# Performance work log

Measured on AMD Instinct MI355X. Metric: run time of the kernel, lower is better.

Reference implementation:

```python
import jax, jax.numpy as jnp
import numpy as np

B, S, E = 2, 2048, 2048
H, HKV, KQV = 16, 4, 2048
D = KQV // H            # 128 head dim
KV_DIM = D * HKV        # 512
WINDOW = 256
NEG = jnp.finfo(jnp.float32).min


def setup_inputs() -> dict:
    key = jax.random.key(0)
    ks = jax.random.split(key, 5)
    sc = 0.02
    return {
        "hidden_states": jax.random.normal(ks[0], (B, S, E), jnp.float32),
        "Wq": jax.random.normal(ks[1], (KQV, E), jnp.float32) * sc,
        "Wk": jax.random.normal(ks[2], (KV_DIM, E), jnp.float32) * sc,
        "Wv": jax.random.normal(ks[3], (KV_DIM, E), jnp.float32) * sc,
        "Wo": jax.random.normal(ks[4], (E, KQV), jnp.float32) * sc,
        "bo": jnp.zeros((E,), jnp.float32),
    }


def reference(hidden_states, Wq, Wk, Wv, Wo, bo):
    x = hidden_states
    # projections (nn.Linear: x @ W.T)
    q = (x @ Wq.T).reshape(B, S, H, D).transpose(0, 2, 1, 3)      # [B,H,S,D]
    k = (x @ Wk.T).reshape(B, S, HKV, D).transpose(0, 2, 1, 3)    # [B,HKV,S,D]
    v = (x @ Wv.T).reshape(B, S, HKV, D).transpose(0, 2, 1, 3)

    # faithful reproduction of the module's index_select head expansion:
    # group_sizes are uniform (H % HKV == 0); both query and kv indices are
    # [0]*g + [1]*g + ... so query head i (i < HKV) is duplicated g times.
    idx = jnp.repeat(jnp.arange(HKV), H // HKV)                   # [H]
    qs = q[:, idx]                                                # [B,H,S,D]
    ks = k[:, idx]
    vs = v[:, idx]

    # GPT-Neo style: no 1/sqrt(D) scaling
    scores = jnp.einsum('bhqd,bhkd->bhqk', qs, ks)                # [B,H,S,S]

    i = jnp.arange(S)[:, None]
    j = jnp.arange(S)[None, :]
    # local causal mask: j <= i and j > i - WINDOW
    mask = (j <= i) & (j > i - WINDOW)                            # [S,S]
    scores = jnp.where(mask[None, None], scores, NEG)
    attn = jax.nn.softmax(scores, axis=-1)

    out = jnp.einsum('bhqk,bhkd->bhqd', attn, vs)                 # [B,H,S,D]
    out = out.transpose(0, 2, 1, 3).reshape(B, S, H * D)          # merge heads
    return out @ Wo.T + bo
```

## Files before the change

kernel.cpp:

```cpp
#include <hip/hip_runtime.h>

typedef _Float16 f16;
typedef _Float16 f16x8 __attribute__((ext_vector_type(8)));
typedef _Float16 f16x4 __attribute__((ext_vector_type(4)));
typedef float    f32x4 __attribute__((ext_vector_type(4)));


__device__ __forceinline__ void load_lds16(const void* g, void* l) {
    __builtin_amdgcn_global_load_lds(
        (__attribute__((address_space(1))) void*)(g),
        (__attribute__((address_space(3))) void*)(l), 16, 0, 0);
}

__global__ __launch_bounds__(256)
void cvt_pack(const float* __restrict__ X, const float* __restrict__ Wq,
              const float* __restrict__ Wk, const float* __restrict__ Wv,
              const float* __restrict__ Wo,
              f16* __restrict__ Xp, f16* __restrict__ Wp, f16* __restrict__ Wrp)
{
    const int blk = blockIdx.x, tid = threadIdx.x;
    if (blk < 4096) {
        int cid = blk * 256 + tid;
        int tile = cid >> 8, wc = cid & 255;
        int row = wc >> 2, kc = wc & 3;
        int m = ((tile >> 6) << 6) + row;
        int t = tile & 63;
        int sk = t * 32 + ((kc ^ ((row >> 1) & 3)) << 3);
        const float* s = X + (size_t)m * 2048 + sk;
        float4 a = *(const float4*)(s);
        float4 b = *(const float4*)(s + 4);
        f16x8 o;
        o[0]=(f16)a.x; o[1]=(f16)a.y; o[2]=(f16)a.z; o[3]=(f16)a.w;
        o[4]=(f16)b.x; o[5]=(f16)b.y; o[6]=(f16)b.z; o[7]=(f16)b.w;
        *(f16x8*)(Xp + (size_t)cid * 8) = o;
    } else if (blk < 5632) {
        int wid = (blk - 4096) * 256 + tid;
        int tile = wid >> 9, wc = wid & 511;
        int row = wc >> 2, kc = wc & 3;
        int n = ((tile >> 6) << 7) + row;
        int t = tile & 63;
        int sk = t * 32 + ((kc ^ ((row >> 1) & 3)) << 3);
        const float* src = (n < 512)  ? (Wq + (size_t)n * 2048 + sk)
                         : (n < 1024) ? (Wk + (size_t)(n - 512) * 2048 + sk)
                                      : (Wv + (size_t)(n - 1024) * 2048 + sk);
        float4 a = *(const float4*)(src);
        float4 b = *(const float4*)(src + 4);
        f16x8 o;
        o[0]=(f16)a.x; o[1]=(f16)a.y; o[2]=(f16)a.z; o[3]=(f16)a.w;
        o[4]=(f16)b.x; o[5]=(f16)b.y; o[6]=(f16)b.z; o[7]=(f16)b.w;
        *(f16x8*)(Wp + (size_t)wid * 8) = o;
    } else {
        int rid = (blk - 5632) * 256 + tid;
        int tile = rid >> 9, wc = rid & 511;
        int row = wc >> 2, kc = wc & 3;
        int e = ((tile >> 4) << 7) + row;
        int t = tile & 15;
        int cc = kc ^ ((row >> 1) & 3);
        int c = t * 32 + (cc << 3);
        int g = c >> 7, d0 = c & 127;
        const float* src = Wo + (size_t)e * 2048 + g * 512 + d0;
        float4 a0 = *(const float4*)(src);
        float4 a1 = *(const float4*)(src + 128);
        float4 a2 = *(const float4*)(src + 256);
        float4 a3 = *(const float4*)(src + 384);
        float4 b0 = *(const float4*)(src + 4);
        float4 b1 = *(const float4*)(src + 132);
        float4 b2 = *(const float4*)(src + 260);
        float4 b3 = *(const float4*)(src + 388);
        f16x8 o;
        o[0] = (f16)(a0.x + a1.x + a2.x + a3.x);
        o[1] = (f16)(a0.y + a1.y + a2.y + a3.y);
        o[2] = (f16)(a0.z + a1.z + a2.z + a3.z);
        o[3] = (f16)(a0.w + a1.w + a2.w + a3.w);
        o[4] = (f16)(b0.x + b1.x + b2.x + b3.x);
        o[5] = (f16)(b0.y + b1.y + b2.y + b3.y);
        o[6] = (f16)(b0.z + b1.z + b2.z + b3.z);
        o[7] = (f16)(b0.w + b1.w + b2.w + b3.w);
        *(f16x8*)(Wrp + (size_t)rid * 8) = o;
    }
}

#define STAGE3(t, buf)                                          \
    {                                                           \
        load_lds16(gs0 + (size_t)(t) * st0, &S[buf][lo0]);      \
        load_lds16(gs1 + (size_t)(t) * st1, &S[buf][lo1]);      \
        load_lds16(gs2 + (size_t)(t) * st2, &S[buf][lo2]);      \
    }

#define PIPE_WAIT(t, NSTEP)                                              \
    if ((t) < (NSTEP)-2) {                                               \
        asm volatile("s_waitcnt vmcnt(6) lgkmcnt(0)" ::: "memory");      \
    } else if ((t) == (NSTEP)-2) {                                       \
        asm volatile("s_waitcnt vmcnt(3) lgkmcnt(0)" ::: "memory");      \
    } else {                                                             \
        asm volatile("s_waitcnt vmcnt(0) lgkmcnt(0)" ::: "memory");      \
    }                                                                    \
    __builtin_amdgcn_s_barrier();

__global__ __launch_bounds__(256)
void qkv_gemm(const f16* __restrict__ Xp, const f16* __restrict__ Wp,
              f16* __restrict__ Qo, f16* __restrict__ Ko, f16* __restrict__ Vo)
{
    const int NSTEP = 64;
    __shared__ __align__(16) f16 S[4][6144];

    const int tid = threadIdx.x;
    const int wave = tid >> 6, lane = tid & 63;
    const int lrow = lane & 15, lquad = lane >> 4;
    const int wr = wave >> 1, wc = wave & 1;

    int id = (int)blockIdx.x;
    int id2 = (id & 7) * 96 + (id >> 3);
    int bx = id2 % 12, by = id2 / 12;
    const int m0 = by * 64, n0 = bx * 128;

    const f16* gs0; const f16* gs1; const f16* gs2;
    size_t st0, st1, st2;
    int lo0, lo1, lo2;
    {
        int sb;
        sb = (wave * 3 + 0) * 64; lo0 = (sb + lane) * 8;
        if (sb < 256) { gs0 = Xp + (size_t)by * 131072 + lo0;          st0 = 2048; }
        else          { gs0 = Wp + (size_t)bx * 262144 + (lo0 - 2048); st0 = 4096; }
        sb = (wave * 3 + 1) * 64; lo1 = (sb + lane) * 8;
        if (sb < 256) { gs1 = Xp + (size_t)by * 131072 + lo1;          st1 = 2048; }
        else          { gs1 = Wp + (size_t)bx * 262144 + (lo1 - 2048); st1 = 4096; }
        sb = (wave * 3 + 2) * 64; lo2 = (sb + lane) * 8;
        if (sb < 256) { gs2 = Xp + (size_t)by * 131072 + lo2;          st2 = 2048; }
        else          { gs2 = Wp + (size_t)bx * 262144 + (lo2 - 2048); st2 = 4096; }
    }

    int aoff[2], boff[4];
#pragma unroll
    for (int t = 0; t < 2; t++) {
        int ra = wr * 32 + t * 16 + lrow;
        aoff[t] = ra * 32 + ((lquad ^ ((ra >> 1) & 3)) << 3);
    }
#pragma unroll
    for (int t = 0; t < 4; t++) {
        int rb = wc * 64 + t * 16 + lrow;
        boff[t] = 2048 + rb * 32 + ((lquad ^ ((rb >> 1) & 3)) << 3);
    }

    f32x4 acc[2][4];
    const f32x4 z4 = {0.f, 0.f, 0.f, 0.f};
#pragma unroll
    for (int i = 0; i < 2; i++) for (int j = 0; j < 4; j++) acc[i][j] = z4;

    STAGE3(0, 0); STAGE3(1, 1); STAGE3(2, 2);

    int buf = 0;
    for (int t = 0; t < NSTEP; ++t) {
        PIPE_WAIT(t, NSTEP);
        if (t < NSTEP - 3) STAGE3(t + 3, (buf + 3) & 3);
        f16x8 af[2], bf[4];
#pragma unroll
        for (int mt = 0; mt < 2; mt++) af[mt] = *(const f16x8*)(&S[buf][aoff[mt]]);
#pragma unroll
        for (int nt = 0; nt < 4; nt++) bf[nt] = *(const f16x8*)(&S[buf][boff[nt]]);
#pragma unroll
        for (int mt = 0; mt < 2; mt++)
#pragma unroll
            for (int nt = 0; nt < 4; nt++)
                acc[mt][nt] = __builtin_amdgcn_mfma_f32_16x16x32_f16(af[mt], bf[nt], acc[mt][nt], 0, 0, 0);
        buf = (buf + 1) & 3;
    }

    const int z = n0 >> 9;
    const int hh = (n0 >> 7) & 3;
    if (z < 2) {
        f16* C = z ? Ko : Qo;
#pragma unroll
        for (int mt = 0; mt < 2; mt++) {
            int mbase = m0 + wr * 32 + mt * 16 + lquad * 4;
#pragma unroll
            for (int r = 0; r < 4; r++) {
                int m = mbase + r;
                int bb = m >> 11, s = m & 2047;
#pragma unroll
                for (int nt = 0; nt < 4; nt++) {
                    int d = wc * 64 + nt * 16 + lrow;
                    C[(size_t)(((bb * 4 + hh) << 11) + s) * 128 + d] = (f16)acc[mt][nt][r];
                }
            }
        }
    } else {
#pragma unroll
        for (int mt = 0; mt < 2; mt++) {
            int mbase = m0 + wr * 32 + mt * 16 + lquad * 4;
            int bb = mbase >> 11, s = mbase & 2047;
#pragma unroll
            for (int nt = 0; nt < 4; nt++) {
                int d = wc * 64 + nt * 16 + lrow;
                f16x4 pk;
#pragma unroll
                for (int r = 0; r < 4; r++) pk[r] = (f16)acc[mt][nt][r];
                *(f16x4*)(Vo + ((size_t)((bb * 4 + hh) * 128 + d) << 11) + s) = pk;
            }
        }
    }
}

__global__ __launch_bounds__(64)
void attn_win(const f16* __restrict__ Q, const f16* __restrict__ Kc,
              const f16* __restrict__ Vt, f16* __restrict__ AO)
{
    const int bg = blockIdx.y;
    const int b = bg >> 2, g = bg & 3;
    const int qbase = blockIdx.x * 16;
    const int lane = threadIdx.x;
    const int lrow = lane & 15, lquad = lane >> 4;

    const f16* Qb = Q  + (size_t)(b * 4 + g) * (2048 * 128);
    const f16* Kb = Kc + (size_t)(b * 4 + g) * (2048 * 128);
    const f16* Vb = Vt + (size_t)(b * 4 + g) * (128 * 2048);

    __shared__ __align__(16) f16 Pl[16 * 128];

    f16x8 qf[4];
    for (int ks = 0; ks < 4; ks++)
        qf[ks] = *(const f16x8*)(Qb + (size_t)(qbase + lrow) * 128 + ks * 32 + lquad * 8);

    float m_i[4], l_i[4];
    f32x4 oa[8];
    const f32x4 z4 = {0.f, 0.f, 0.f, 0.f};
    for (int r = 0; r < 4; r++) { m_i[r] = -30000.f; l_i[r] = 0.f; }
    for (int nt = 0; nt < 8; nt++) oa[nt] = z4;

    const int t0 = (qbase >= 256) ? (((qbase - 255) >> 7) << 7) : 0;
    for (int kt = t0; kt <= qbase + 15; kt += 128) {
        f32x4 sc[8];
        for (int nt = 0; nt < 8; nt++) sc[nt] = z4;
        for (int nt = 0; nt < 8; nt++) {
            for (int ks = 0; ks < 4; ks++) {
                f16x8 kf = *(const f16x8*)(Kb + (size_t)(kt + nt * 16 + lrow) * 128 + ks * 32 + lquad * 8);
                sc[nt] = __builtin_amdgcn_mfma_f32_16x16x32_f16(qf[ks], kf, sc[nt], 0, 0, 0);
            }
        }
        for (int r = 0; r < 4; r++) {
            const int qi = qbase + lquad * 4 + r;
            float rmax = -60000.f;
            for (int nt = 0; nt < 8; nt++) {
                int kj = kt + nt * 16 + lrow;
                float sval = sc[nt][r];
                bool ok = (kj <= qi) && (kj + 256 > qi);
                sval = ok ? sval : -60000.f;
                sc[nt][r] = sval;
                rmax = fmaxf(rmax, sval);
            }
            rmax = fmaxf(rmax, __shfl_xor(rmax, 1));
            rmax = fmaxf(rmax, __shfl_xor(rmax, 2));
            rmax = fmaxf(rmax, __shfl_xor(rmax, 4));
            rmax = fmaxf(rmax, __shfl_xor(rmax, 8));
            float mold = m_i[r];
            float mnew = fmaxf(mold, rmax);
            float alpha = __expf(mold - mnew);
            m_i[r] = mnew;
            float rsum = 0.f;
            for (int nt = 0; nt < 8; nt++) {
                float p = __expf(sc[nt][r] - mnew);
                sc[nt][r] = p;
                rsum += p;
            }
            rsum += __shfl_xor(rsum, 1);
            rsum += __shfl_xor(rsum, 2);
            rsum += __shfl_xor(rsum, 4);
            rsum += __shfl_xor(rsum, 8);
            l_i[r] = l_i[r] * alpha + rsum;
            for (int nt = 0; nt < 8; nt++) oa[nt][r] *= alpha;
        }
        for (int nt = 0; nt < 8; nt++)
            for (int r = 0; r < 4; r++)
                Pl[(lquad * 4 + r) * 128 + nt * 16 + lrow] = (f16)sc[nt][r];
        __syncthreads();
        f16x8 pf[4];
        for (int ks = 0; ks < 4; ks++)
            pf[ks] = *(const f16x8*)(Pl + lrow * 128 + ks * 32 + lquad * 8);
        for (int nt = 0; nt < 8; nt++) {
            for (int ks = 0; ks < 4; ks++) {
                f16x8 vf = *(const f16x8*)(Vb + (size_t)(nt * 16 + lrow) * 2048 + kt + ks * 32 + lquad * 8);
                oa[nt] = __builtin_amdgcn_mfma_f32_16x16x32_f16(pf[ks], vf, oa[nt], 0, 0, 0);
            }
        }
        __syncthreads();
    }
    float inv[4];
    for (int r = 0; r < 4; r++) inv[r] = (l_i[r] > 0.f) ? 1.f / l_i[r] : 0.f;
    for (int nt = 0; nt < 8; nt++) {
        for (int r = 0; r < 4; r++) {
            int q = qbase + lquad * 4 + r;
            int d = nt * 16 + lrow;
            int m = b * 2048 + q;
            int col = g * 128 + d;
            int p = m >> 6, r2 = m & 63;
            int t = col >> 5;
            int cc = (col >> 3) & 3;
            size_t off = (((size_t)p * 16 + t) * 64 + r2) * 32
                       + ((cc ^ ((r2 >> 1) & 3)) << 3) + (col & 7);
            AO[off] = (f16)(oa[nt][r] * inv[r]);
        }
    }
}

__global__ __launch_bounds__(256)
void out_gemm(const f16* __restrict__ Ap, const f16* __restrict__ Bp,
              const float* __restrict__ bias, float* __restrict__ C)
{
    const int NSTEP = 16, N = 2048;
    __shared__ __align__(16) f16 S[4][6144];

    const int tid = threadIdx.x;
    const int wave = tid >> 6, lane = tid & 63;
    const int lrow = lane & 15, lquad = lane >> 4;
    const int wr = wave >> 1, wc = wave & 1;

    int id = (int)blockIdx.x;
    int id2 = (id & 7) * 128 + (id >> 3);
    int bx = id2 & 15, by = id2 >> 4;
    const int m0 = by * 64, n0 = bx * 128;

    const f16* gs0; const f16* gs1; const f16* gs2;
    size_t st0, st1, st2;
    int lo0, lo1, lo2;
    {
        int sb;
        sb = (wave * 3 + 0) * 64; lo0 = (sb + lane) * 8;
        if (sb < 256) { gs0 = Ap + (size_t)by * 32768 + lo0;          st0 = 2048; }
        else          { gs0 = Bp + (size_t)bx * 65536 + (lo0 - 2048); st0 = 4096; }
        sb = (wave * 3 + 1) * 64; lo1 = (sb + lane) * 8;
        if (sb < 256) { gs1 = Ap + (size_t)by * 32768 + lo1;          st1 = 2048; }
        else          { gs1 = Bp + (size_t)bx * 65536 + (lo1 - 2048); st1 = 4096; }
        sb = (wave * 3 + 2) * 64; lo2 = (sb + lane) * 8;
        if (sb < 256) { gs2 = Ap + (size_t)by * 32768 + lo2;          st2 = 2048; }
        else          { gs2 = Bp + (size_t)bx * 65536 + (lo2 - 2048); st2 = 4096; }
    }

    int aoff[2], boff[4];
#pragma unroll
    for (int t = 0; t < 2; t++) {
        int ra = wr * 32 + t * 16 + lrow;
        aoff[t] = ra * 32 + ((lquad ^ ((ra >> 1) & 3)) << 3);
    }
#pragma unroll
    for (int t = 0; t < 4; t++) {
        int rb = wc * 64 + t * 16 + lrow;
        boff[t] = 2048 + rb * 32 + ((lquad ^ ((rb >> 1) & 3)) << 3);
    }

    f32x4 acc[2][4];
    const f32x4 z4 = {0.f, 0.f, 0.f, 0.f};
#pragma unroll
    for (int i = 0; i < 2; i++) for (int j = 0; j < 4; j++) acc[i][j] = z4;

    STAGE3(0, 0); STAGE3(1, 1); STAGE3(2, 2);

    int buf = 0;
    for (int t = 0; t < NSTEP; ++t) {
        PIPE_WAIT(t, NSTEP);
        if (t < NSTEP - 3) STAGE3(t + 3, (buf + 3) & 3);
        f16x8 af[2], bf[4];
#pragma unroll
        for (int mt = 0; mt < 2; mt++) af[mt] = *(const f16x8*)(&S[buf][aoff[mt]]);
#pragma unroll
        for (int nt = 0; nt < 4; nt++) bf[nt] = *(const f16x8*)(&S[buf][boff[nt]]);
#pragma unroll
        for (int mt = 0; mt < 2; mt++)
#pragma unroll
            for (int nt = 0; nt < 4; nt++)
                acc[mt][nt] = __builtin_amdgcn_mfma_f32_16x16x32_f16(af[mt], bf[nt], acc[mt][nt], 0, 0, 0);
        buf = (buf + 1) & 3;
    }

#pragma unroll
    for (int nt = 0; nt < 4; nt++) {
        int n = n0 + wc * 64 + nt * 16 + lrow;
        float bv2 = bias[n];
#pragma unroll
        for (int mt = 0; mt < 2; mt++) {
            int mbase = m0 + wr * 32 + mt * 16 + lquad * 4;
#pragma unroll
            for (int r = 0; r < 4; r++)
                C[(size_t)(mbase + r) * N + n] = acc[mt][nt][r] + bv2;
        }
    }
}

extern "C" void kernel_launch(void* const* d_in, const int* in_sizes, int n_in,
                              void* d_out, int out_size, void* d_ws, size_t ws_size,
                              hipStream_t stream)
{
    const float* x  = (const float*)d_in[0];
    const float* Wq = (const float*)d_in[1];
    const float* Wk = (const float*)d_in[2];
    const float* Wv = (const float*)d_in[3];
    const float* Wo = (const float*)d_in[4];
    const float* bo = (const float*)d_in[5];
    float* out = (float*)d_out;

    f16* Xp  = (f16*)d_ws;
    f16* AO  = Xp;
    f16* Wp  = Xp  + 8388608;
    f16* Wrp = Wp  + 3145728;
    f16* Qws = Wrp + 1048576;
    f16* Kws = Qws + 2097152;
    f16* Vws = Kws + 2097152;

    cvt_pack<<<dim3(6144), 256, 0, stream>>>(x, Wq, Wk, Wv, Wo, Xp, Wp, Wrp);
    qkv_gemm<<<dim3(768), 256, 0, stream>>>(Xp, Wp, Qws, Kws, Vws);
    attn_win<<<dim3(128, 8), 64, 0, stream>>>(Qws, Kws, Vws, AO);
    out_gemm<<<dim3(1024), 256, 0, stream>>>(AO, Wrp, bo, out);
}
```

Measured before the change: 202.5 us.

## Stage K/V tiles in LDS with double buffering across four-wave attention blocks

The QKV GEMM epilogue now writes K and V in per-128-key tiles with an XOR-swizzled layout. The attention kernel uses 256-thread blocks covering 64 queries, so the four waves share each K/V tile. Tiles are loaded into LDS with async global_load_lds and double buffered, and the P tile is swizzled per wave. This replaces the redundant per-wave global reads of K and V, at the cost of 144KB+ of LDS per block, which limits occupancy, and fewer blocks (256).

```diff
diff --git a/kernel.cpp b/kernel.cpp
--- a/kernel.cpp
+++ b/kernel.cpp
@@ -168,8 +168,7 @@
 
     const int z = n0 >> 9;
     const int hh = (n0 >> 7) & 3;
-    if (z < 2) {
-        f16* C = z ? Ko : Qo;
+    if (z == 0) {
 #pragma unroll
         for (int mt = 0; mt < 2; mt++) {
             int mbase = m0 + wr * 32 + mt * 16 + lquad * 4;
@@ -180,7 +179,24 @@
 #pragma unroll
                 for (int nt = 0; nt < 4; nt++) {
                     int d = wc * 64 + nt * 16 + lrow;
-                    C[(size_t)(((bb * 4 + hh) << 11) + s) * 128 + d] = (f16)acc[mt][nt][r];
+                    Qo[(size_t)(((bb * 4 + hh) << 11) + s) * 128 + d] = (f16)acc[mt][nt][r];
+                }
+            }
+        }
+    } else if (z == 1) {
+#pragma unroll
+        for (int mt = 0; mt < 2; mt++) {
+            int mbase = m0 + wr * 32 + mt * 16 + lquad * 4;
+#pragma unroll
+            for (int r = 0; r < 4; r++) {
+                int m = mbase + r;
+                int bb = m >> 11, s = m & 2047;
+                size_t base = ((size_t)(bb * 4 + hh) * 16 + (s >> 7)) * 16384
+                            + (size_t)(s & 127) * 128;
+#pragma unroll
+                for (int nt = 0; nt < 4; nt++) {
+                    int d = wc * 64 + nt * 16 + lrow;
+                    Ko[base + (((d >> 3) ^ (s & 15)) << 3) + (d & 7)] = (f16)acc[mt][nt][r];
                 }
             }
         }
@@ -189,57 +205,102 @@
         for (int mt = 0; mt < 2; mt++) {
             int mbase = m0 + wr * 32 + mt * 16 + lquad * 4;
             int bb = mbase >> 11, s = mbase & 2047;
+            int tt = s >> 7, sl = s & 127;
+            int gsx = sl >> 3, j0 = sl & 7;
 #pragma unroll
             for (int nt = 0; nt < 4; nt++) {
                 int d = wc * 64 + nt * 16 + lrow;
                 f16x4 pk;
 #pragma unroll
                 for (int r = 0; r < 4; r++) pk[r] = (f16)acc[mt][nt][r];
-                *(f16x4*)(Vo + ((size_t)((bb * 4 + hh) * 128 + d) << 11) + s) = pk;
-            }
-        }
-    }
-}
-
-__global__ __launch_bounds__(64)
-void attn_win(const f16* __restrict__ Q, const f16* __restrict__ Kc,
-              const f16* __restrict__ Vt, f16* __restrict__ AO)
+                *(f16x4*)(Vo + ((size_t)(bb * 4 + hh) * 16 + tt) * 16384
+                             + (size_t)d * 128 + ((gsx ^ (d & 15)) << 3) + j0) = pk;
+            }
+        }
+    }
+}
+
+__global__ __launch_bounds__(256)
+void attn_win(const f16* __restrict__ Q, const f16* __restrict__ Kp,
+              const f16* __restrict__ Vp, f16* __restrict__ AO)
 {
-    const int bg = blockIdx.y;
+    const int h = blockIdx.x;
+    const int bg = h & 7, qt = h >> 3;
     const int b = bg >> 2, g = bg & 3;
-    const int qbase = blockIdx.x * 16;
-    const int lane = threadIdx.x;
+    const int qbase = qt * 64;
+    const int tid = threadIdx.x;
+    const int wave = tid >> 6, lane = tid & 63;
     const int lrow = lane & 15, lquad = lane >> 4;
-
-    const f16* Qb = Q  + (size_t)(b * 4 + g) * (2048 * 128);
-    const f16* Kb = Kc + (size_t)(b * 4 + g) * (2048 * 128);
-    const f16* Vb = Vt + (size_t)(b * 4 + g) * (128 * 2048);
-
-    __shared__ __align__(16) f16 Pl[16 * 128];
+    const int qw = qbase + wave * 16;
+
+    const f16* Qb = Q  + (size_t)bg * (2048 * 128);
+    const f16* Kt = Kp + (size_t)bg * (2048 * 128);
+    const f16* Vt = Vp + (size_t)bg * (2048 * 128);
+
+    __shared__ __align__(16) f16 Ks[2][16384];
+    __shared__ __align__(16) f16 Vs[2][16384];
+    __shared__ __align__(16) f16 Pl[4][2048];
 
     f16x8 qf[4];
+#pragma unroll
     for (int ks = 0; ks < 4; ks++)
-        qf[ks] = *(const f16x8*)(Qb + (size_t)(qbase + lrow) * 128 + ks * 32 + lquad * 8);
+        qf[ks] = *(const f16x8*)(Qb + (size_t)(qw + lrow) * 128 + ks * 32 + lquad * 8);
 
     float m_i[4], l_i[4];
     f32x4 oa[8];
     const f32x4 z4 = {0.f, 0.f, 0.f, 0.f};
+#pragma unroll
     for (int r = 0; r < 4; r++) { m_i[r] = -30000.f; l_i[r] = 0.f; }
+#pragma unroll
     for (int nt = 0; nt < 8; nt++) oa[nt] = z4;
 
-    const int t0 = (qbase >= 256) ? (((qbase - 255) >> 7) << 7) : 0;
-    for (int kt = t0; kt <= qbase + 15; kt += 128) {
+    const int tstart = (qbase >= 256) ? ((qbase - 255) >> 7) : 0;
+    const int tend = (qbase + 63) >> 7;
+
+    {
+        const f16* ksrc = Kt + (size_t)tstart * 16384;
+        const f16* vsrc = Vt + (size_t)tstart * 16384;
+#pragma unroll
+        for (int j = 0; j < 8; j++) {
+            load_lds16(ksrc + (j * 256 + tid) * 8, &Ks[0][(j * 256 + tid) * 8]);
+            load_lds16(vsrc + (j * 256 + tid) * 8, &Vs[0][(j * 256 + tid) * 8]);
+        }
+    }
+
+    int buf = 0;
+    for (int t = tstart; t <= tend; ++t) {
+        if (t < tend) {
+            const f16* ksrc = Kt + (size_t)(t + 1) * 16384;
+            const f16* vsrc = Vt + (size_t)(t + 1) * 16384;
+#pragma unroll
+            for (int j = 0; j < 8; j++) {
+                load_lds16(ksrc + (j * 256 + tid) * 8, &Ks[buf ^ 1][(j * 256 + tid) * 8]);
+                load_lds16(vsrc + (j * 256 + tid) * 8, &Vs[buf ^ 1][(j * 256 + tid) * 8]);
+            }
+            asm volatile("s_waitcnt vmcnt(16)" ::: "memory");
+        } else {
+            asm volatile("s_waitcnt vmcnt(0)" ::: "memory");
+        }
+        __builtin_amdgcn_s_barrier();
+
+        const int kt = t * 128;
         f32x4 sc[8];
+#pragma unroll
         for (int nt = 0; nt < 8; nt++) sc[nt] = z4;
+#pragma unroll
         for (int nt = 0; nt < 8; nt++) {
+#pragma unroll
             for (int ks = 0; ks < 4; ks++) {
-                f16x8 kf = *(const f16x8*)(Kb + (size_t)(kt + nt * 16 + lrow) * 128 + ks * 32 + lquad * 8);
+                f16x8 kf = *(const f16x8*)(&Ks[buf][(nt * 16 + lrow) * 128
+                                  + (((ks * 4 + lquad) ^ lrow) << 3)]);
                 sc[nt] = __builtin_amdgcn_mfma_f32_16x16x32_f16(qf[ks], kf, sc[nt], 0, 0, 0);
             }
         }
+#pragma unroll
         for (int r = 0; r < 4; r++) {
-            const int qi = qbase + lquad * 4 + r;
+            const int qi = qw + lquad * 4 + r;
             float rmax = -60000.f;
+#pragma unroll
             for (int nt = 0; nt < 8; nt++) {
                 int kj = kt + nt * 16 + lrow;
                 float sval = sc[nt][r];
@@ -257,6 +318,7 @@
             float alpha = __expf(mold - mnew);
             m_i[r] = mnew;
             float rsum = 0.f;
+#pragma unroll
             for (int nt = 0; nt < 8; nt++) {
                 float p = __expf(sc[nt][r] - mnew);
                 sc[nt][r] = p;
@@ -267,35 +329,51 @@
             rsum += __shfl_xor(rsum, 4);
             rsum += __shfl_xor(rsum, 8);
             l_i[r] = l_i[r] * alpha + rsum;
+#pragma unroll
             for (int nt = 0; nt < 8; nt++) oa[nt][r] *= alpha;
         }
+#pragma unroll
         for (int nt = 0; nt < 8; nt++)
-            for (int r = 0; r < 4; r++)
-                Pl[(lquad * 4 + r) * 128 + nt * 16 + lrow] = (f16)sc[nt][r];
-        __syncthreads();
+#pragma unroll
+            for (int r = 0; r < 4; r++) {
+                int row = lquad * 4 + r;
+                int col = nt * 16 + lrow;
+                Pl[wave][row * 128 + (((col >> 3) ^ row) << 3) + (col & 7)] = (f16)sc[nt][r];
+            }
         f16x8 pf[4];
+#pragma unroll
         for (int ks = 0; ks < 4; ks++)
-            pf[ks] = *(const f16x8*)(Pl + lrow * 128 + ks * 32 + lquad * 8);
+            pf[ks] = *(const f16x8*)(&Pl[wave][lrow * 128
+                              + (((ks * 4 + lquad) ^ lrow) << 3)]);
+#pragma unroll
         for (int nt = 0; nt < 8; nt++) {
+#pragma unroll
             for (int ks = 0; ks < 4; ks++) {
-                f16x8 vf = *(const f16x8*)(Vb + (size_t)(nt * 16 + lrow) * 2048 + kt + ks * 32 + lquad * 8);
+                f16x8 vf = *(const f16x8*)(&Vs[buf][(nt * 16 + lrow) * 128
+                                  + (((ks * 4 + lquad) ^ lrow) << 3)]);
                 oa[nt] = __builtin_amdgcn_mfma_f32_16x16x32_f16(pf[ks], vf, oa[nt], 0, 0, 0);
             }
         }
-        __syncthreads();
-    }
+        asm volatile("s_waitcnt lgkmcnt(0)" ::: "memory");
+        __builtin_amdgcn_s_barrier();
+        buf ^= 1;
+    }
+
     float inv[4];
+#pragma unroll
     for (int r = 0; r < 4; r++) inv[r] = (l_i[r] > 0.f) ? 1.f / l_i[r] : 0.f;
+#pragma unroll
     for (int nt = 0; nt < 8; nt++) {
+#pragma unroll
         for (int r = 0; r < 4; r++) {
-            int q = qbase + lquad * 4 + r;
+            int q = qw + lquad * 4 + r;
             int d = nt * 16 + lrow;
             int m = b * 2048 + q;
             int col = g * 128 + d;
             int p = m >> 6, r2 = m & 63;
-            int t = col >> 5;
+            int tt = col >> 5;
             int cc = (col >> 3) & 3;
-            size_t off = (((size_t)p * 16 + t) * 64 + r2) * 32
+            size_t off = (((size_t)p * 16 + tt) * 64 + r2) * 32
                        + ((cc ^ ((r2 >> 1) & 3)) << 3) + (col & 7);
             AO[off] = (f16)(oa[nt][r] * inv[r]);
         }
@@ -407,6 +485,6 @@
 
     cvt_pack<<<dim3(6144), 256, 0, stream>>>(x, Wq, Wk, Wv, Wo, Xp, Wp, Wrp);
     qkv_gemm<<<dim3(768), 256, 0, stream>>>(Xp, Wp, Qws, Kws, Vws);
-    attn_win<<<dim3(128, 8), 64, 0, stream>>>(Qws, Kws, Vws, AO);
+    attn_win<<<dim3(256), 256, 0, stream>>>(Qws, Kws, Vws, AO);
     out_gemm<<<dim3(1024), 256, 0, stream>>>(AO, Wrp, bo, out);
 }
```

Result: faster. 177.7 us (-12.3%).
